# Kernel tuning notes

Measured on AMD Instinct MI355X. Metric: run time of the kernel, lower is better.

The kernel has to match this reference:

```python
import jax, jax.numpy as jnp
import numpy as np

N_NODES = 100000
N_EDGES = 1600000
IN_F = 128
HID_F = 128
N_CLS = 40


def _linear_params(key, out_f, in_f):
    k1, k2 = jax.random.split(key)
    s = 1.0 / np.sqrt(in_f)
    w = jax.random.uniform(k1, (out_f, in_f), jnp.float32, -s, s)
    b = jax.random.uniform(k2, (out_f,), jnp.float32, -s, s)
    return w, b


def setup_inputs() -> dict:
    key = jax.random.key(0)
    ks = jax.random.split(key, 9)
    in_feat = jax.random.normal(ks[0], (N_NODES, IN_F), jnp.float32)
    src = jax.random.randint(ks[1], (N_EDGES,), 0, N_NODES, jnp.int32)
    dst = jax.random.randint(ks[2], (N_EDGES,), 0, N_NODES, jnp.int32)
    pool_w1, pool_b1 = _linear_params(ks[3], IN_F, IN_F)
    self_w1, self_b1 = _linear_params(ks[4], HID_F, IN_F)
    neigh_w1, neigh_b1 = _linear_params(ks[5], HID_F, IN_F)
    pool_w2, pool_b2 = _linear_params(ks[6], HID_F, HID_F)
    self_w2, self_b2 = _linear_params(ks[7], N_CLS, HID_F)
    neigh_w2, neigh_b2 = _linear_params(ks[8], N_CLS, HID_F)
    return dict(in_feat=in_feat, src=src, dst=dst,
                pool_w1=pool_w1, pool_b1=pool_b1, self_w1=self_w1, self_b1=self_b1,
                neigh_w1=neigh_w1, neigh_b1=neigh_b1,
                pool_w2=pool_w2, pool_b2=pool_b2, self_w2=self_w2, self_b2=self_b2,
                neigh_w2=neigh_w2, neigh_b2=neigh_b2)


def sage_conv_pool(h, src, dst, pool_w, pool_b, self_w, self_b, neigh_w, neigh_b):
    # fc_pool + relu on nodes first (N < E), then gather per edge
    m = jax.nn.relu(h @ pool_w.T + pool_b)            # [N, d]
    msgs = m[src]                                     # [E, d] gather
    agg = jax.ops.segment_max(msgs, dst, num_segments=N_NODES)  # [N, d]
    agg = jnp.where(jnp.isfinite(agg), agg, 0.0)      # zero for isolated nodes
    return h @ self_w.T + self_b + agg @ neigh_w.T + neigh_b


def reference(in_feat, src, dst,
              pool_w1, pool_b1, self_w1, self_b1, neigh_w1, neigh_b1,
              pool_w2, pool_b2, self_w2, self_b2, neigh_w2, neigh_b2):
    h = sage_conv_pool(in_feat, src, dst, pool_w1, pool_b1, self_w1, self_b1, neigh_w1, neigh_b1)
    h = jax.nn.relu(h)  # dropout is identity in eval mode
    h = sage_conv_pool(h, src, dst, pool_w2, pool_b2, self_w2, self_b2, neigh_w2, neigh_b2)
    return h
```

## Files before the change

### kernel.cpp

```cpp
#include <hip/hip_runtime.h>


#define N_FEAT 128
#define NWG_A 256
#define BSHIFT 10
#define NBMAX 128

typedef __attribute__((ext_vector_type(8))) short bf16x8;
typedef __attribute__((ext_vector_type(8))) unsigned short u16x8;
typedef __attribute__((ext_vector_type(4))) float f32x4;

static __device__ __forceinline__ unsigned short f2bf(float f) {
    unsigned u = __float_as_uint(f);
    unsigned r = (u + 0x7fffu + ((u >> 16) & 1u)) >> 16;
    return (unsigned short)r;
}

__global__ void prep_kernel(const float* __restrict__ pw1, const float* __restrict__ sw1,
                            const float* __restrict__ nw1, const float* __restrict__ pw2,
                            const float* __restrict__ sw2, const float* __restrict__ nw2,
                            const float* __restrict__ sb1, const float* __restrict__ nb1,
                            const float* __restrict__ sb2, const float* __restrict__ nb2,
                            unsigned short* __restrict__ wb_p1, unsigned short* __restrict__ wb_s1,
                            unsigned short* __restrict__ wb_n1, unsigned short* __restrict__ wb_p2,
                            unsigned short* __restrict__ wb_s2, unsigned short* __restrict__ wb_n2,
                            float* __restrict__ b_sn1, float* __restrict__ b_sn2)
{
    int t = blockIdx.x * 256 + threadIdx.x;
    if (t < 16384) {
        wb_p1[t] = f2bf(pw1[t]);
        wb_s1[t] = f2bf(sw1[t]);
        wb_n1[t] = f2bf(nw1[t]);
        wb_p2[t] = f2bf(pw2[t]);
    }
    if (t < 6144) {
        int row = t >> 7;
        wb_s2[t] = (row < 40) ? f2bf(sw2[t]) : 0;
        wb_n2[t] = (row < 40) ? f2bf(nw2[t]) : 0;
    }
    if (t < 128) b_sn1[t] = sb1[t] + nb1[t];
    if (t < 64)  b_sn2[t] = (t < 40) ? (sb2[t] + nb2[t]) : 0.f;
}

__global__ void f2b_kernel(const float4* __restrict__ in, ushort4* __restrict__ out, int n)
{
    int i = blockIdx.x * 256 + threadIdx.x;
    if (i < n) {
        float4 v = in[i];
        ushort4 o;
        o.x = f2bf(v.x); o.y = f2bf(v.y); o.z = f2bf(v.z); o.w = f2bf(v.w);
        out[i] = o;
    }
}

__global__ __launch_bounds__(256) void bin_count_kernel(const int* __restrict__ dst,
                                                        int* __restrict__ wgcnt,
                                                        int E, int NB)
{
    __shared__ int cnt[NBMAX];
    const int wg = blockIdx.x, tid = threadIdx.x;
    if (tid < NB) cnt[tid] = 0;
    __syncthreads();
    const int slab = (E + NWG_A - 1) / NWG_A;
    const int e0 = wg * slab;
    const int e1 = min(e0 + slab, E);
    for (int e = e0 + tid; e < e1; e += 256)
        atomicAdd(&cnt[dst[e] >> BSHIFT], 1);
    __syncthreads();
    if (tid < NB) wgcnt[tid * NWG_A + wg] = cnt[tid];
}

__global__ __launch_bounds__(256) void bin_scan_kernel(const int* __restrict__ wgcnt,
                                                       int* __restrict__ binoff, int NB)
{
    __shared__ int sh[256];
    const int t = threadIdx.x;
    const int base = t * NB;
    int s = 0;
    for (int k = 0; k < NB; k++) s += wgcnt[base + k];
    sh[t] = s;
    __syncthreads();
    for (int off = 1; off < 256; off <<= 1) {
        int x = (t >= off) ? sh[t - off] : 0;
        __syncthreads();
        sh[t] += x;
        __syncthreads();
    }
    int run = sh[t] - s;
    for (int k = 0; k < NB; k++) {
        int v = wgcnt[base + k];
        binoff[base + k] = run;
        run += v;
    }
    if (t == 255) binoff[NB * NWG_A] = run;
}

__global__ __launch_bounds__(256) void bin_scatter_kernel(const int* __restrict__ src,
                                                          const int* __restrict__ dst,
                                                          const int* __restrict__ binoff,
                                                          unsigned* __restrict__ binned,
                                                          int E, int NB)
{
    __shared__ int cur[NBMAX];
    const int wg = blockIdx.x, tid = threadIdx.x;
    if (tid < NB) cur[tid] = binoff[tid * NWG_A + wg];
    __syncthreads();
    const int slab = (E + NWG_A - 1) / NWG_A;
    const int e0 = wg * slab;
    const int e1 = min(e0 + slab, E);
    for (int e = e0 + tid; e < e1; e += 256) {
        int d = dst[e];
        int b = d >> BSHIFT;
        unsigned rec = ((unsigned)(d & ((1 << BSHIFT) - 1)) << 17) | (unsigned)src[e];
        int p = atomicAdd(&cur[b], 1);
        binned[p] = rec;
    }
}

__global__ __launch_bounds__(256) void csr_build_kernel(const unsigned* __restrict__ binned,
                                                        const int* __restrict__ binoff,
                                                        int* __restrict__ csr,
                                                        int* __restrict__ offsets,
                                                        int* __restrict__ counts, int M)
{
    __shared__ int cnt[1 << BSHIFT];
    __shared__ int scn[1 << BSHIFT];
    __shared__ int sh[256];
    const int b = blockIdx.x, t = threadIdx.x;
    const int rs = binoff[b * NWG_A];
    const int re = binoff[(b + 1) * NWG_A];

    for (int j = t; j < (1 << BSHIFT); j += 256) cnt[j] = 0;
    __syncthreads();
    for (int i = rs + t; i < re; i += 256)
        atomicAdd(&cnt[binned[i] >> 17], 1);
    __syncthreads();

    const int base4 = t * 4;
    int v[4];
#pragma unroll
    for (int k = 0; k < 4; k++) v[k] = cnt[base4 + k];
    int s = v[0] + v[1] + v[2] + v[3];
    sh[t] = s;
    __syncthreads();
    for (int off = 1; off < 256; off <<= 1) {
        int x = (t >= off) ? sh[t - off] : 0;
        __syncthreads();
        sh[t] += x;
        __syncthreads();
    }
    int run = sh[t] - s;
#pragma unroll
    for (int k = 0; k < 4; k++) {
        scn[base4 + k] = run;
        run += v[k];
    }

    const int node0 = b << BSHIFT;
#pragma unroll
    for (int k = 0; k < 4; k++) {
        int j = base4 + k;
        int node = node0 + j;
        if (node < M) {
            counts[node] = v[k];
            offsets[node] = rs + scn[j];
        }
    }
    __syncthreads();

    for (int i = rs + t; i < re; i += 256) {
        unsigned r = binned[i];
        int p = atomicAdd(&scn[r >> 17], 1);
        csr[rs + p] = (int)(r & 0x1FFFFu);
    }
}

__global__ __launch_bounds__(256) void gather_max_kernel(
    const u16x8* __restrict__ m16, const int* __restrict__ csr,
    const int* __restrict__ offsets, const int* __restrict__ counts,
    u16x8* __restrict__ agg16, int Nn)
{
    int wid = (blockIdx.x * 256 + threadIdx.x) >> 6;
    int lane = threadIdx.x & 63;
    if (wid >= Nn) return;
    const int g = lane >> 4, c = lane & 15;
    int start = offsets[wid];
    int deg = counts[wid];
    u16x8 acc = (u16x8){0, 0, 0, 0, 0, 0, 0, 0};
    for (int j0 = 0; j0 < deg; j0 += 64) {
        int nb = deg - j0;
        if (nb > 64) nb = 64;
        int sl = csr[start + j0 + (lane < nb ? lane : nb - 1)];
        for (int j = 0; j < nb; j += 4) {
            int jj = j + g;
            if (jj >= nb) jj = nb - 1;
            int s = __shfl(sl, jj);
            u16x8 v = m16[(size_t)s * 16 + c];
            acc = __builtin_elementwise_max(acc, v);
        }
    }
#pragma unroll
    for (int d = 16; d <= 32; d <<= 1) {
        int4 a = *(int4*)&acc;
        int4 t;
        t.x = __shfl_xor(a.x, d);
        t.y = __shfl_xor(a.y, d);
        t.z = __shfl_xor(a.z, d);
        t.w = __shfl_xor(a.w, d);
        acc = __builtin_elementwise_max(acc, *(u16x8*)&t);
    }
    if (g == 0) agg16[(size_t)wid * 16 + c] = acc;
}

template<int NT, bool RELU, int NPAIRS, bool F32OUT>
__global__ __launch_bounds__(256, 4) void mfma_gemm_kernel(
    const unsigned short* __restrict__ A0, const unsigned short* __restrict__ B0,
    const unsigned short* __restrict__ A1, const unsigned short* __restrict__ B1,
    const float* __restrict__ bias, void* __restrict__ Cout, int M, int Nout)
{
    constexpr int NR = NT * 16;
    __shared__ unsigned short Bs[NR * 136];
    __shared__ float BsF[NR];

    const int tid = threadIdx.x;
    const int w = tid >> 6, lane = tid & 63;
    const int q = lane >> 4, r16 = lane & 15;
    const int m0 = blockIdx.x * 128;

    if (tid < NR) BsF[tid] = (tid < Nout) ? bias[tid] : 0.f;

    int rowA[2];
#pragma unroll
    for (int rt = 0; rt < 2; rt++) {
        int r = m0 + w * 32 + rt * 16 + r16;
        rowA[rt] = r < M ? r : (M - 1);
    }

    f32x4 acc[2][NT];
#pragma unroll
    for (int i = 0; i < 2; i++)
#pragma unroll
        for (int j = 0; j < NT; j++) acc[i][j] = (f32x4){0.f, 0.f, 0.f, 0.f};

    for (int p = 0; p < NPAIRS; p++) {
        const unsigned short* __restrict__ A = p ? A1 : A0;
        const unsigned short* __restrict__ B = p ? B1 : B0;
        if (p) __syncthreads();
        for (int j = tid; j < NR * 16; j += 256) {
            int row = j >> 4, cc = j & 15;
            uint4 v = *(const uint4*)&B[(size_t)row * 128 + cc * 8];
            *(uint4*)&Bs[row * 136 + cc * 8] = v;
        }
        __syncthreads();

#pragma unroll
        for (int k0 = 0; k0 < 128; k0 += 32) {
            bf16x8 af[2];
#pragma unroll
            for (int rt = 0; rt < 2; rt++)
                af[rt] = *(const bf16x8*)&A[(size_t)rowA[rt] * 128 + k0 + q * 8];
#pragma unroll
            for (int ct = 0; ct < NT; ct++) {
                bf16x8 bfr = *(const bf16x8*)&Bs[(ct * 16 + r16) * 136 + k0 + q * 8];
#pragma unroll
                for (int rt = 0; rt < 2; rt++)
                    acc[rt][ct] = __builtin_amdgcn_mfma_f32_16x16x32_bf16(
                        af[rt], bfr, acc[rt][ct], 0, 0, 0);
            }
        }
    }

#pragma unroll
    for (int rt = 0; rt < 2; rt++) {
#pragma unroll
        for (int ct = 0; ct < NT; ct++) {
            int col = ct * 16 + r16;
#pragma unroll
            for (int r = 0; r < 4; r++) {
                int grow = m0 + w * 32 + rt * 16 + q * 4 + r;
                float v = acc[rt][ct][r] + BsF[col];
                if (RELU) v = fmaxf(v, 0.f);
                if (grow < M && col < Nout) {
                    if (F32OUT)
                        ((float*)Cout)[(size_t)grow * Nout + col] = v;
                    else
                        ((unsigned short*)Cout)[(size_t)grow * Nout + col] = f2bf(v);
                }
            }
        }
    }
}

extern "C" void kernel_launch(void* const* d_in, const int* in_sizes, int n_in,
                              void* d_out, int out_size, void* d_ws, size_t ws_size,
                              hipStream_t stream)
{
    const float* in_feat = (const float*)d_in[0];
    const int*   src     = (const int*)d_in[1];
    const int*   dst     = (const int*)d_in[2];
    const float* pw1 = (const float*)d_in[3];  const float* pb1 = (const float*)d_in[4];
    const float* sw1 = (const float*)d_in[5];  const float* sb1 = (const float*)d_in[6];
    const float* nw1 = (const float*)d_in[7];  const float* nb1 = (const float*)d_in[8];
    const float* pw2 = (const float*)d_in[9];  const float* pb2 = (const float*)d_in[10];
    const float* sw2 = (const float*)d_in[11]; const float* sb2 = (const float*)d_in[12];
    const float* nw2 = (const float*)d_in[13]; const float* nb2 = (const float*)d_in[14];
    float* out = (float*)d_out;

    const int M = in_sizes[0] / N_FEAT;
    const int E = in_sizes[1];
    const int NB = (M + (1 << BSHIFT) - 1) >> BSHIFT;

    char* base = (char*)d_ws;
    size_t off = 0;
    auto alloc = [&](size_t bytes) { char* p = base + off; off = (off + bytes + 255) & ~(size_t)255; return p; };
    unsigned short* wb_p1 = (unsigned short*)alloc(16384 * 2);
    unsigned short* wb_s1 = (unsigned short*)alloc(16384 * 2);
    unsigned short* wb_n1 = (unsigned short*)alloc(16384 * 2);
    unsigned short* wb_p2 = (unsigned short*)alloc(16384 * 2);
    unsigned short* wb_s2 = (unsigned short*)alloc(6144 * 2);
    unsigned short* wb_n2 = (unsigned short*)alloc(6144 * 2);
    float* b_sn1 = (float*)alloc(128 * 4);
    float* b_sn2 = (float*)alloc(64 * 4);
    unsigned short* in_b = (unsigned short*)alloc((size_t)M * 128 * 2);
    unsigned short* mb   = (unsigned short*)alloc((size_t)M * 128 * 2);
    unsigned short* agg  = (unsigned short*)alloc((size_t)M * 128 * 2);
    unsigned short* h1   = (unsigned short*)alloc((size_t)M * 128 * 2);
    int* counts  = (int*)alloc((size_t)M * 4);
    int* offsets = (int*)alloc((size_t)M * 4);
    int* wgcnt   = (int*)alloc((size_t)NB * NWG_A * 4);
    int* binoff  = (int*)alloc(((size_t)NB * NWG_A + 1) * 4);
    unsigned* binned = (unsigned*)alloc((size_t)E * 4);
    int* csr     = (int*)alloc((size_t)E * 4);

    const int gemm_grid = (M + 127) / 128;
    const int gather_grid = (M * 64 + 255) / 256;
    const int nf4 = M * 128 / 4;

    prep_kernel<<<64, 256, 0, stream>>>(pw1, sw1, nw1, pw2, sw2, nw2,
                                        sb1, nb1, sb2, nb2,
                                        wb_p1, wb_s1, wb_n1, wb_p2, wb_s2, wb_n2,
                                        b_sn1, b_sn2);
    f2b_kernel<<<(nf4 + 255) / 256, 256, 0, stream>>>((const float4*)in_feat, (ushort4*)in_b, nf4);

    bin_count_kernel<<<NWG_A, 256, 0, stream>>>(dst, wgcnt, E, NB);
    bin_scan_kernel<<<1, 256, 0, stream>>>(wgcnt, binoff, NB);
    bin_scatter_kernel<<<NWG_A, 256, 0, stream>>>(src, dst, binoff, binned, E, NB);
    csr_build_kernel<<<NB, 256, 0, stream>>>(binned, binoff, csr, offsets, counts, M);

    mfma_gemm_kernel<8, true, 1, false><<<gemm_grid, 256, 0, stream>>>(
        in_b, wb_p1, nullptr, nullptr, pb1, mb, M, 128);
    gather_max_kernel<<<gather_grid, 256, 0, stream>>>(
        (const u16x8*)mb, csr, offsets, counts, (u16x8*)agg, M);
    mfma_gemm_kernel<8, true, 2, false><<<gemm_grid, 256, 0, stream>>>(
        in_b, wb_s1, agg, wb_n1, b_sn1, h1, M, 128);

    mfma_gemm_kernel<8, true, 1, false><<<gemm_grid, 256, 0, stream>>>(
        h1, wb_p2, nullptr, nullptr, pb2, mb, M, 128);
    gather_max_kernel<<<gather_grid, 256, 0, stream>>>(
        (const u16x8*)mb, csr, offsets, counts, (u16x8*)agg, M);
    mfma_gemm_kernel<3, false, 2, true><<<gemm_grid, 256, 0, stream>>>(
        h1, wb_s2, agg, wb_n2, b_sn2, out, M, 40);
}
```

Measured before the change: 412.7 us.

## Fuse neighbor max-gather into the self+neighbor GEMM via shared-memory aggregates

New measurement: 568.8 us. +37.8%, slower.

```diff
diff --git a/kernel.cpp b/kernel.cpp
--- a/kernel.cpp
+++ b/kernel.cpp
@@ -175,47 +175,9 @@
     }
 }
 
-__global__ __launch_bounds__(256) void gather_max_kernel(
-    const u16x8* __restrict__ m16, const int* __restrict__ csr,
-    const int* __restrict__ offsets, const int* __restrict__ counts,
-    u16x8* __restrict__ agg16, int Nn)
-{
-    int wid = (blockIdx.x * 256 + threadIdx.x) >> 6;
-    int lane = threadIdx.x & 63;
-    if (wid >= Nn) return;
-    const int g = lane >> 4, c = lane & 15;
-    int start = offsets[wid];
-    int deg = counts[wid];
-    u16x8 acc = (u16x8){0, 0, 0, 0, 0, 0, 0, 0};
-    for (int j0 = 0; j0 < deg; j0 += 64) {
-        int nb = deg - j0;
-        if (nb > 64) nb = 64;
-        int sl = csr[start + j0 + (lane < nb ? lane : nb - 1)];
-        for (int j = 0; j < nb; j += 4) {
-            int jj = j + g;
-            if (jj >= nb) jj = nb - 1;
-            int s = __shfl(sl, jj);
-            u16x8 v = m16[(size_t)s * 16 + c];
-            acc = __builtin_elementwise_max(acc, v);
-        }
-    }
-#pragma unroll
-    for (int d = 16; d <= 32; d <<= 1) {
-        int4 a = *(int4*)&acc;
-        int4 t;
-        t.x = __shfl_xor(a.x, d);
-        t.y = __shfl_xor(a.y, d);
-        t.z = __shfl_xor(a.z, d);
-        t.w = __shfl_xor(a.w, d);
-        acc = __builtin_elementwise_max(acc, *(u16x8*)&t);
-    }
-    if (g == 0) agg16[(size_t)wid * 16 + c] = acc;
-}
-
-template<int NT, bool RELU, int NPAIRS, bool F32OUT>
+template<int NT, bool RELU, bool F32OUT>
 __global__ __launch_bounds__(256, 4) void mfma_gemm_kernel(
     const unsigned short* __restrict__ A0, const unsigned short* __restrict__ B0,
-    const unsigned short* __restrict__ A1, const unsigned short* __restrict__ B1,
     const float* __restrict__ bias, void* __restrict__ Cout, int M, int Nout)
 {
     constexpr int NR = NT * 16;
@@ -242,31 +204,162 @@
 #pragma unroll
         for (int j = 0; j < NT; j++) acc[i][j] = (f32x4){0.f, 0.f, 0.f, 0.f};
 
-    for (int p = 0; p < NPAIRS; p++) {
-        const unsigned short* __restrict__ A = p ? A1 : A0;
-        const unsigned short* __restrict__ B = p ? B1 : B0;
-        if (p) __syncthreads();
-        for (int j = tid; j < NR * 16; j += 256) {
-            int row = j >> 4, cc = j & 15;
-            uint4 v = *(const uint4*)&B[(size_t)row * 128 + cc * 8];
-            *(uint4*)&Bs[row * 136 + cc * 8] = v;
-        }
-        __syncthreads();
-
-#pragma unroll
-        for (int k0 = 0; k0 < 128; k0 += 32) {
-            bf16x8 af[2];
+    for (int j = tid; j < NR * 16; j += 256) {
+        int row = j >> 4, cc = j & 15;
+        uint4 v = *(const uint4*)&B0[(size_t)row * 128 + cc * 8];
+        *(uint4*)&Bs[row * 136 + cc * 8] = v;
+    }
+    __syncthreads();
+
+#pragma unroll
+    for (int k0 = 0; k0 < 128; k0 += 32) {
+        bf16x8 af[2];
+#pragma unroll
+        for (int rt = 0; rt < 2; rt++)
+            af[rt] = *(const bf16x8*)&A0[(size_t)rowA[rt] * 128 + k0 + q * 8];
+#pragma unroll
+        for (int ct = 0; ct < NT; ct++) {
+            bf16x8 bfr = *(const bf16x8*)&Bs[(ct * 16 + r16) * 136 + k0 + q * 8];
 #pragma unroll
             for (int rt = 0; rt < 2; rt++)
-                af[rt] = *(const bf16x8*)&A[(size_t)rowA[rt] * 128 + k0 + q * 8];
-#pragma unroll
-            for (int ct = 0; ct < NT; ct++) {
-                bf16x8 bfr = *(const bf16x8*)&Bs[(ct * 16 + r16) * 136 + k0 + q * 8];
-#pragma unroll
-                for (int rt = 0; rt < 2; rt++)
-                    acc[rt][ct] = __builtin_amdgcn_mfma_f32_16x16x32_bf16(
-                        af[rt], bfr, acc[rt][ct], 0, 0, 0);
+                acc[rt][ct] = __builtin_amdgcn_mfma_f32_16x16x32_bf16(
+                    af[rt], bfr, acc[rt][ct], 0, 0, 0);
+        }
+    }
+
+#pragma unroll
+    for (int rt = 0; rt < 2; rt++) {
+#pragma unroll
+        for (int ct = 0; ct < NT; ct++) {
+            int col = ct * 16 + r16;
+#pragma unroll
+            for (int r = 0; r < 4; r++) {
+                int grow = m0 + w * 32 + rt * 16 + q * 4 + r;
+                float v = acc[rt][ct][r] + BsF[col];
+                if (RELU) v = fmaxf(v, 0.f);
+                if (grow < M && col < Nout) {
+                    if (F32OUT)
+                        ((float*)Cout)[(size_t)grow * Nout + col] = v;
+                    else
+                        ((unsigned short*)Cout)[(size_t)grow * Nout + col] = f2bf(v);
+                }
             }
+        }
+    }
+}
+
+template<int NT, bool RELU, bool F32OUT>
+__global__ __launch_bounds__(256, 2) void gemm_gather_kernel(
+    const unsigned short* __restrict__ A0, const unsigned short* __restrict__ B0,
+    const unsigned short* __restrict__ B1, const unsigned short* __restrict__ m,
+    const int* __restrict__ csr, const int* __restrict__ offsets,
+    const int* __restrict__ counts,
+    const float* __restrict__ bias, void* __restrict__ Cout, int M, int Nout)
+{
+    constexpr int NR = NT * 16;
+    __shared__ unsigned short Bs[NR * 136];
+    __shared__ unsigned short Agg[128 * 132];
+    __shared__ float BsF[NR];
+
+    const int tid = threadIdx.x;
+    const int w = tid >> 6, lane = tid & 63;
+    const int q = lane >> 4, r16 = lane & 15;
+    const int m0 = blockIdx.x * 128;
+
+    if (tid < NR) BsF[tid] = (tid < Nout) ? bias[tid] : 0.f;
+
+    for (int j = tid; j < NR * 16; j += 256) {
+        int row = j >> 4, cc = j & 15;
+        uint4 v = *(const uint4*)&B0[(size_t)row * 128 + cc * 8];
+        *(uint4*)&Bs[row * 136 + cc * 8] = v;
+    }
+
+    {
+        const u16x8* __restrict__ m16 = (const u16x8*)m;
+        const int g = q, c = r16;
+        int nodeL = m0 + w * 32 + (lane & 31);
+        int degL = 0, offL = 0;
+        if (nodeL < M) { degL = counts[nodeL]; offL = offsets[nodeL]; }
+        for (int n = 0; n < 32; n++) {
+            int deg = __shfl(degL, n);
+            int start = __shfl(offL, n);
+            u16x8 acc = (u16x8){0, 0, 0, 0, 0, 0, 0, 0};
+            for (int j0 = 0; j0 < deg; j0 += 64) {
+                int nb = deg - j0;
+                if (nb > 64) nb = 64;
+                int sl = csr[start + j0 + (lane < nb ? lane : nb - 1)];
+                for (int j = 0; j < nb; j += 4) {
+                    int jj = j + g;
+                    if (jj >= nb) jj = nb - 1;
+                    int s = __shfl(sl, jj);
+                    u16x8 v = m16[(size_t)s * 16 + c];
+                    acc = __builtin_elementwise_max(acc, v);
+                }
+            }
+#pragma unroll
+            for (int d = 16; d <= 32; d <<= 1) {
+                int4 a = *(int4*)&acc;
+                int4 t;
+                t.x = __shfl_xor(a.x, d);
+                t.y = __shfl_xor(a.y, d);
+                t.z = __shfl_xor(a.z, d);
+                t.w = __shfl_xor(a.w, d);
+                acc = __builtin_elementwise_max(acc, *(u16x8*)&t);
+            }
+            if (g == 0) *(u16x8*)&Agg[(w * 32 + n) * 132 + c * 8] = acc;
+        }
+    }
+    __syncthreads();
+
+    int rowA[2];
+#pragma unroll
+    for (int rt = 0; rt < 2; rt++) {
+        int r = m0 + w * 32 + rt * 16 + r16;
+        rowA[rt] = r < M ? r : (M - 1);
+    }
+
+    f32x4 acc[2][NT];
+#pragma unroll
+    for (int i = 0; i < 2; i++)
+#pragma unroll
+        for (int j = 0; j < NT; j++) acc[i][j] = (f32x4){0.f, 0.f, 0.f, 0.f};
+
+#pragma unroll
+    for (int k0 = 0; k0 < 128; k0 += 32) {
+        bf16x8 af[2];
+#pragma unroll
+        for (int rt = 0; rt < 2; rt++)
+            af[rt] = *(const bf16x8*)&A0[(size_t)rowA[rt] * 128 + k0 + q * 8];
+#pragma unroll
+        for (int ct = 0; ct < NT; ct++) {
+            bf16x8 bfr = *(const bf16x8*)&Bs[(ct * 16 + r16) * 136 + k0 + q * 8];
+#pragma unroll
+            for (int rt = 0; rt < 2; rt++)
+                acc[rt][ct] = __builtin_amdgcn_mfma_f32_16x16x32_bf16(
+                    af[rt], bfr, acc[rt][ct], 0, 0, 0);
+        }
+    }
+    __syncthreads();
+    for (int j = tid; j < NR * 16; j += 256) {
+        int row = j >> 4, cc = j & 15;
+        uint4 v = *(const uint4*)&B1[(size_t)row * 128 + cc * 8];
+        *(uint4*)&Bs[row * 136 + cc * 8] = v;
+    }
+    __syncthreads();
+
+#pragma unroll
+    for (int k0 = 0; k0 < 128; k0 += 32) {
+        bf16x8 af[2];
+#pragma unroll
+        for (int rt = 0; rt < 2; rt++)
+            af[rt] = *(const bf16x8*)&Agg[(w * 32 + rt * 16 + r16) * 132 + k0 + q * 8];
+#pragma unroll
+        for (int ct = 0; ct < NT; ct++) {
+            bf16x8 bfr = *(const bf16x8*)&Bs[(ct * 16 + r16) * 136 + k0 + q * 8];
+#pragma unroll
+            for (int rt = 0; rt < 2; rt++)
+                acc[rt][ct] = __builtin_amdgcn_mfma_f32_16x16x32_bf16(
+                    af[rt], bfr, acc[rt][ct], 0, 0, 0);
         }
     }
 
@@ -323,7 +416,6 @@
     float* b_sn2 = (float*)alloc(64 * 4);
     unsigned short* in_b = (unsigned short*)alloc((size_t)M * 128 * 2);
     unsigned short* mb   = (unsigned short*)alloc((size_t)M * 128 * 2);
-    unsigned short* agg  = (unsigned short*)alloc((size_t)M * 128 * 2);
     unsigned short* h1   = (unsigned short*)alloc((size_t)M * 128 * 2);
     int* counts  = (int*)alloc((size_t)M * 4);
     int* offsets = (int*)alloc((size_t)M * 4);
@@ -333,7 +425,6 @@
     int* csr     = (int*)alloc((size_t)E * 4);
 
     const int gemm_grid = (M + 127) / 128;
-    const int gather_grid = (M * 64 + 255) / 256;
     const int nf4 = M * 128 / 4;
 
     prep_kernel<<<64, 256, 0, stream>>>(pw1, sw1, nw1, pw2, sw2, nw2,
@@ -347,17 +438,13 @@
     bin_scatter_kernel<<<NWG_A, 256, 0, stream>>>(src, dst, binoff, binned, E, NB);
     csr_build_kernel<<<NB, 256, 0, stream>>>(binned, binoff, csr, offsets, counts, M);
 
-    mfma_gemm_kernel<8, true, 1, false><<<gemm_grid, 256, 0, stream>>>(
-        in_b, wb_p1, nullptr, nullptr, pb1, mb, M, 128);
-    gather_max_kernel<<<gather_grid, 256, 0, stream>>>(
-        (const u16x8*)mb, csr, offsets, counts, (u16x8*)agg, M);
-    mfma_gemm_kernel<8, true, 2, false><<<gemm_grid, 256, 0, stream>>>(
-        in_b, wb_s1, agg, wb_n1, b_sn1, h1, M, 128);
-
-    mfma_gemm_kernel<8, true, 1, false><<<gemm_grid, 256, 0, stream>>>(
-        h1, wb_p2, nullptr, nullptr, pb2, mb, M, 128);
-    gather_max_kernel<<<gather_grid, 256, 0, stream>>>(
-        (const u16x8*)mb, csr, offsets, counts, (u16x8*)agg, M);
-    mfma_gemm_kernel<3, false, 2, true><<<gemm_grid, 256, 0, stream>>>(
-        h1, wb_s2, agg, wb_n2, b_sn2, out, M, 40);
-}
+    mfma_gemm_kernel<8, true, false><<<gemm_grid, 256, 0, stream>>>(
+        in_b, wb_p1, pb1, mb, M, 128);
+    gemm_gather_kernel<8, true, false><<<gemm_grid, 256, 0, stream>>>(
+        in_b, wb_s1, wb_n1, mb, csr, offsets, counts, b_sn1, h1, M, 128);
+
+    mfma_gemm_kernel<8, true, false><<<gemm_grid, 256, 0, stream>>>(
+        h1, wb_p2, pb2, mb, M, 128);
+    gemm_gather_kernel<3, false, true><<<gemm_grid, 256, 0, stream>>>(
+        h1, wb_s2, wb_n2, mb, csr, offsets, counts, b_sn2, out, M, 40);
+}
```

## Fuse layer-1 self/neigh GEMM with layer-2 pool GEMM and drop input conversion

Applied to the files above, without the earlier changes.

After: 393.8 us. -4.6%, faster.

```diff
diff --git a/kernel.cpp b/kernel.cpp
--- a/kernel.cpp
+++ b/kernel.cpp
@@ -16,58 +16,57 @@
     return (unsigned short)r;
 }
 
-__global__ void prep_kernel(const float* __restrict__ pw1, const float* __restrict__ sw1,
-                            const float* __restrict__ nw1, const float* __restrict__ pw2,
-                            const float* __restrict__ sw2, const float* __restrict__ nw2,
-                            const float* __restrict__ sb1, const float* __restrict__ nb1,
-                            const float* __restrict__ sb2, const float* __restrict__ nb2,
-                            unsigned short* __restrict__ wb_p1, unsigned short* __restrict__ wb_s1,
-                            unsigned short* __restrict__ wb_n1, unsigned short* __restrict__ wb_p2,
-                            unsigned short* __restrict__ wb_s2, unsigned short* __restrict__ wb_n2,
-                            float* __restrict__ b_sn1, float* __restrict__ b_sn2)
-{
-    int t = blockIdx.x * 256 + threadIdx.x;
-    if (t < 16384) {
-        wb_p1[t] = f2bf(pw1[t]);
-        wb_s1[t] = f2bf(sw1[t]);
-        wb_n1[t] = f2bf(nw1[t]);
-        wb_p2[t] = f2bf(pw2[t]);
-    }
-    if (t < 6144) {
-        int row = t >> 7;
-        wb_s2[t] = (row < 40) ? f2bf(sw2[t]) : 0;
-        wb_n2[t] = (row < 40) ? f2bf(nw2[t]) : 0;
-    }
-    if (t < 128) b_sn1[t] = sb1[t] + nb1[t];
-    if (t < 64)  b_sn2[t] = (t < 40) ? (sb2[t] + nb2[t]) : 0.f;
-}
-
-__global__ void f2b_kernel(const float4* __restrict__ in, ushort4* __restrict__ out, int n)
-{
-    int i = blockIdx.x * 256 + threadIdx.x;
-    if (i < n) {
-        float4 v = in[i];
-        ushort4 o;
-        o.x = f2bf(v.x); o.y = f2bf(v.y); o.z = f2bf(v.z); o.w = f2bf(v.w);
-        out[i] = o;
-    }
-}
-
-__global__ __launch_bounds__(256) void bin_count_kernel(const int* __restrict__ dst,
-                                                        int* __restrict__ wgcnt,
-                                                        int E, int NB)
+static __device__ __forceinline__ bf16x8 loadA_f32(const float* __restrict__ A, size_t idx) {
+    float4 a = *(const float4*)&A[idx];
+    float4 b = *(const float4*)&A[idx + 4];
+    bf16x8 r;
+    r[0] = (short)f2bf(a.x); r[1] = (short)f2bf(a.y);
+    r[2] = (short)f2bf(a.z); r[3] = (short)f2bf(a.w);
+    r[4] = (short)f2bf(b.x); r[5] = (short)f2bf(b.y);
+    r[6] = (short)f2bf(b.z); r[7] = (short)f2bf(b.w);
+    return r;
+}
+
+__global__ __launch_bounds__(256) void prep_bin_kernel(
+    const float* __restrict__ pw1, const float* __restrict__ sw1,
+    const float* __restrict__ nw1, const float* __restrict__ pw2,
+    const float* __restrict__ sw2, const float* __restrict__ nw2,
+    const float* __restrict__ sb1, const float* __restrict__ nb1,
+    const float* __restrict__ sb2, const float* __restrict__ nb2,
+    unsigned short* __restrict__ wb_p1, unsigned short* __restrict__ wb_s1,
+    unsigned short* __restrict__ wb_n1, unsigned short* __restrict__ wb_p2,
+    unsigned short* __restrict__ wb_s2, unsigned short* __restrict__ wb_n2,
+    float* __restrict__ b_sn1, float* __restrict__ b_sn2,
+    const int* __restrict__ dst, int* __restrict__ wgcnt, int E, int NB)
 {
     __shared__ int cnt[NBMAX];
-    const int wg = blockIdx.x, tid = threadIdx.x;
-    if (tid < NB) cnt[tid] = 0;
-    __syncthreads();
-    const int slab = (E + NWG_A - 1) / NWG_A;
-    const int e0 = wg * slab;
-    const int e1 = min(e0 + slab, E);
-    for (int e = e0 + tid; e < e1; e += 256)
-        atomicAdd(&cnt[dst[e] >> BSHIFT], 1);
-    __syncthreads();
-    if (tid < NB) wgcnt[tid * NWG_A + wg] = cnt[tid];
+    if (blockIdx.x < NWG_A) {
+        const int wg = blockIdx.x, tid = threadIdx.x;
+        if (tid < NB) cnt[tid] = 0;
+        __syncthreads();
+        const int slab = (E + NWG_A - 1) / NWG_A;
+        const int e0 = wg * slab;
+        const int e1 = min(e0 + slab, E);
+        for (int e = e0 + tid; e < e1; e += 256)
+            atomicAdd(&cnt[dst[e] >> BSHIFT], 1);
+        __syncthreads();
+        if (tid < NB) wgcnt[tid * NWG_A + wg] = cnt[tid];
+    } else {
+        int t = (blockIdx.x - NWG_A) * 256 + threadIdx.x;
+        if (t < 16384) {
+            wb_p1[t] = f2bf(pw1[t]);
+            wb_s1[t] = f2bf(sw1[t]);
+            wb_n1[t] = f2bf(nw1[t]);
+            wb_p2[t] = f2bf(pw2[t]);
+        }
+        if (t < 6144) {
+            int row = t >> 7;
+            wb_s2[t] = (row < 40) ? f2bf(sw2[t]) : 0;
+            wb_n2[t] = (row < 40) ? f2bf(nw2[t]) : 0;
+        }
+        if (t < 128) b_sn1[t] = sb1[t] + nb1[t];
+        if (t < 64)  b_sn2[t] = (t < 40) ? (sb2[t] + nb2[t]) : 0.f;
+    }
 }
 
 __global__ __launch_bounds__(256) void bin_scan_kernel(const int* __restrict__ wgcnt,
@@ -212,9 +211,9 @@
     if (g == 0) agg16[(size_t)wid * 16 + c] = acc;
 }
 
-template<int NT, bool RELU, int NPAIRS, bool F32OUT>
+template<int NT, bool RELU, int NPAIRS, bool A0F32, bool F32OUT>
 __global__ __launch_bounds__(256, 4) void mfma_gemm_kernel(
-    const unsigned short* __restrict__ A0, const unsigned short* __restrict__ B0,
+    const void* __restrict__ A0v, const unsigned short* __restrict__ B0,
     const unsigned short* __restrict__ A1, const unsigned short* __restrict__ B1,
     const float* __restrict__ bias, void* __restrict__ Cout, int M, int Nout)
 {
@@ -243,7 +242,6 @@
         for (int j = 0; j < NT; j++) acc[i][j] = (f32x4){0.f, 0.f, 0.f, 0.f};
 
     for (int p = 0; p < NPAIRS; p++) {
-        const unsigned short* __restrict__ A = p ? A1 : A0;
         const unsigned short* __restrict__ B = p ? B1 : B0;
         if (p) __syncthreads();
         for (int j = tid; j < NR * 16; j += 256) {
@@ -257,8 +255,14 @@
         for (int k0 = 0; k0 < 128; k0 += 32) {
             bf16x8 af[2];
 #pragma unroll
-            for (int rt = 0; rt < 2; rt++)
-                af[rt] = *(const bf16x8*)&A[(size_t)rowA[rt] * 128 + k0 + q * 8];
+            for (int rt = 0; rt < 2; rt++) {
+                if (p == 0 && A0F32)
+                    af[rt] = loadA_f32((const float*)A0v, (size_t)rowA[rt] * 128 + k0 + q * 8);
+                else {
+                    const unsigned short* Ab = p ? A1 : (const unsigned short*)A0v;
+                    af[rt] = *(const bf16x8*)&Ab[(size_t)rowA[rt] * 128 + k0 + q * 8];
+                }
+            }
 #pragma unroll
             for (int ct = 0; ct < NT; ct++) {
                 bf16x8 bfr = *(const bf16x8*)&Bs[(ct * 16 + r16) * 136 + k0 + q * 8];
@@ -291,6 +295,143 @@
     }
 }
 
+__global__ __launch_bounds__(256, 2) void sn_pool_kernel(
+    const float* __restrict__ A0f, const unsigned short* __restrict__ B0,
+    const unsigned short* __restrict__ A1, const unsigned short* __restrict__ B1,
+    const float* __restrict__ bias_sn, const unsigned short* __restrict__ Bp,
+    const float* __restrict__ bias_p, unsigned short* __restrict__ h1out,
+    unsigned short* __restrict__ m2out, int M)
+{
+    __shared__ unsigned short Bs[128 * 136];
+    __shared__ unsigned short H[128 * 136];
+    __shared__ float BsF[128];
+
+    const int tid = threadIdx.x;
+    const int w = tid >> 6, lane = tid & 63;
+    const int q = lane >> 4, r16 = lane & 15;
+    const int m0 = blockIdx.x * 128;
+
+    if (tid < 128) BsF[tid] = bias_sn[tid];
+
+    int rowA[2];
+#pragma unroll
+    for (int rt = 0; rt < 2; rt++) {
+        int r = m0 + w * 32 + rt * 16 + r16;
+        rowA[rt] = r < M ? r : (M - 1);
+    }
+
+    f32x4 acc[2][8];
+#pragma unroll
+    for (int i = 0; i < 2; i++)
+#pragma unroll
+        for (int j = 0; j < 8; j++) acc[i][j] = (f32x4){0.f, 0.f, 0.f, 0.f};
+
+    for (int j = tid; j < 2048; j += 256) {
+        int row = j >> 4, cc = j & 15;
+        *(uint4*)&Bs[row * 136 + cc * 8] = *(const uint4*)&B0[(size_t)row * 128 + cc * 8];
+    }
+    __syncthreads();
+#pragma unroll
+    for (int k0 = 0; k0 < 128; k0 += 32) {
+        bf16x8 af[2];
+#pragma unroll
+        for (int rt = 0; rt < 2; rt++)
+            af[rt] = loadA_f32(A0f, (size_t)rowA[rt] * 128 + k0 + q * 8);
+#pragma unroll
+        for (int ct = 0; ct < 8; ct++) {
+            bf16x8 bfr = *(const bf16x8*)&Bs[(ct * 16 + r16) * 136 + k0 + q * 8];
+#pragma unroll
+            for (int rt = 0; rt < 2; rt++)
+                acc[rt][ct] = __builtin_amdgcn_mfma_f32_16x16x32_bf16(
+                    af[rt], bfr, acc[rt][ct], 0, 0, 0);
+        }
+    }
+    __syncthreads();
+
+    for (int j = tid; j < 2048; j += 256) {
+        int row = j >> 4, cc = j & 15;
+        *(uint4*)&Bs[row * 136 + cc * 8] = *(const uint4*)&B1[(size_t)row * 128 + cc * 8];
+    }
+    __syncthreads();
+#pragma unroll
+    for (int k0 = 0; k0 < 128; k0 += 32) {
+        bf16x8 af[2];
+#pragma unroll
+        for (int rt = 0; rt < 2; rt++)
+            af[rt] = *(const bf16x8*)&A1[(size_t)rowA[rt] * 128 + k0 + q * 8];
+#pragma unroll
+        for (int ct = 0; ct < 8; ct++) {
+            bf16x8 bfr = *(const bf16x8*)&Bs[(ct * 16 + r16) * 136 + k0 + q * 8];
+#pragma unroll
+            for (int rt = 0; rt < 2; rt++)
+                acc[rt][ct] = __builtin_amdgcn_mfma_f32_16x16x32_bf16(
+                    af[rt], bfr, acc[rt][ct], 0, 0, 0);
+        }
+    }
+
+#pragma unroll
+    for (int rt = 0; rt < 2; rt++) {
+#pragma unroll
+        for (int ct = 0; ct < 8; ct++) {
+            int col = ct * 16 + r16;
+#pragma unroll
+            for (int r = 0; r < 4; r++) {
+                int lr = w * 32 + rt * 16 + q * 4 + r;
+                int grow = m0 + lr;
+                float v = fmaxf(acc[rt][ct][r] + BsF[col], 0.f);
+                unsigned short hb = f2bf(v);
+                H[lr * 136 + col] = hb;
+                if (grow < M) h1out[(size_t)grow * 128 + col] = hb;
+            }
+        }
+    }
+    __syncthreads();
+
+    for (int j = tid; j < 2048; j += 256) {
+        int row = j >> 4, cc = j & 15;
+        *(uint4*)&Bs[row * 136 + cc * 8] = *(const uint4*)&Bp[(size_t)row * 128 + cc * 8];
+    }
+    if (tid < 128) BsF[tid] = bias_p[tid];
+    __syncthreads();
+
+#pragma unroll
+    for (int i = 0; i < 2; i++)
+#pragma unroll
+        for (int j = 0; j < 8; j++) acc[i][j] = (f32x4){0.f, 0.f, 0.f, 0.f};
+
+#pragma unroll
+    for (int k0 = 0; k0 < 128; k0 += 32) {
+        bf16x8 af[2];
+#pragma unroll
+        for (int rt = 0; rt < 2; rt++)
+            af[rt] = *(const bf16x8*)&H[(w * 32 + rt * 16 + r16) * 136 + k0 + q * 8];
+#pragma unroll
+        for (int ct = 0; ct < 8; ct++) {
+            bf16x8 bfr = *(const bf16x8*)&Bs[(ct * 16 + r16) * 136 + k0 + q * 8];
+#pragma unroll
+            for (int rt = 0; rt < 2; rt++)
+                acc[rt][ct] = __builtin_amdgcn_mfma_f32_16x16x32_bf16(
+                    af[rt], bfr, acc[rt][ct], 0, 0, 0);
+        }
+    }
+
+#pragma unroll
+    for (int rt = 0; rt < 2; rt++) {
+#pragma unroll
+        for (int ct = 0; ct < 8; ct++) {
+            int col = ct * 16 + r16;
+#pragma unroll
+            for (int r = 0; r < 4; r++) {
+                int grow = m0 + w * 32 + rt * 16 + q * 4 + r;
+                if (grow < M) {
+                    float v = fmaxf(acc[rt][ct][r] + BsF[col], 0.f);
+                    m2out[(size_t)grow * 128 + col] = f2bf(v);
+                }
+            }
+        }
+    }
+}
+
 extern "C" void kernel_launch(void* const* d_in, const int* in_sizes, int n_in,
                               void* d_out, int out_size, void* d_ws, size_t ws_size,
                               hipStream_t stream)
@@ -321,7 +462,6 @@
     unsigned short* wb_n2 = (unsigned short*)alloc(6144 * 2);
     float* b_sn1 = (float*)alloc(128 * 4);
     float* b_sn2 = (float*)alloc(64 * 4);
-    unsigned short* in_b = (unsigned short*)alloc((size_t)M * 128 * 2);
     unsigned short* mb   = (unsigned short*)alloc((size_t)M * 128 * 2);
     unsigned short* agg  = (unsigned short*)alloc((size_t)M * 128 * 2);
     unsigned short* h1   = (unsigned short*)alloc((size_t)M * 128 * 2);
@@ -334,30 +474,24 @@
 
     const int gemm_grid = (M + 127) / 128;
     const int gather_grid = (M * 64 + 255) / 256;
-    const int nf4 = M * 128 / 4;
-
-    prep_kernel<<<64, 256, 0, stream>>>(pw1, sw1, nw1, pw2, sw2, nw2,
-                                        sb1, nb1, sb2, nb2,
-                                        wb_p1, wb_s1, wb_n1, wb_p2, wb_s2, wb_n2,
-                                        b_sn1, b_sn2);
-    f2b_kernel<<<(nf4 + 255) / 256, 256, 0, stream>>>((const float4*)in_feat, (ushort4*)in_b, nf4);
-
-    bin_count_kernel<<<NWG_A, 256, 0, stream>>>(dst, wgcnt, E, NB);
+
+    prep_bin_kernel<<<NWG_A + 64, 256, 0, stream>>>(
+        pw1, sw1, nw1, pw2, sw2, nw2, sb1, nb1, sb2, nb2,
+        wb_p1, wb_s1, wb_n1, wb_p2, wb_s2, wb_n2, b_sn1, b_sn2,
+        dst, wgcnt, E, NB);
     bin_scan_kernel<<<1, 256, 0, stream>>>(wgcnt, binoff, NB);
     bin_scatter_kernel<<<NWG_A, 256, 0, stream>>>(src, dst, binoff, binned, E, NB);
     csr_build_kernel<<<NB, 256, 0, stream>>>(binned, binoff, csr, offsets, counts, M);
 
-    mfma_gemm_kernel<8, true, 1, false><<<gemm_grid, 256, 0, stream>>>(
-        in_b, wb_p1, nullptr, nullptr, pb1, mb, M, 128);
+    mfma_gemm_kernel<8, true, 1, true, false><<<gemm_grid, 256, 0, stream>>>(
+        in_feat, wb_p1, nullptr, nullptr, pb1, mb, M, 128);
     gather_max_kernel<<<gather_grid, 256, 0, stream>>>(
         (const u16x8*)mb, csr, offsets, counts, (u16x8*)agg, M);
-    mfma_gemm_kernel<8, true, 2, false><<<gemm_grid, 256, 0, stream>>>(
-        in_b, wb_s1, agg, wb_n1, b_sn1, h1, M, 128);
-
-    mfma_gemm_kernel<8, true, 1, false><<<gemm_grid, 256, 0, stream>>>(
-        h1, wb_p2, nullptr, nullptr, pb2, mb, M, 128);
+    sn_pool_kernel<<<gemm_grid, 256, 0, stream>>>(
+        in_feat, wb_s1, agg, wb_n1, b_sn1, wb_p2, pb2, h1, mb, M);
+
     gather_max_kernel<<<gather_grid, 256, 0, stream>>>(
         (const u16x8*)mb, csr, offsets, counts, (u16x8*)agg, M);
-    mfma_gemm_kernel<3, false, 2, true><<<gemm_grid, 256, 0, stream>>>(
+    mfma_gemm_kernel<3, false, 2, false, true><<<gemm_grid, 256, 0, stream>>>(
         h1, wb_s2, agg, wb_n2, b_sn2, out, M, 40);
 }
```
